# Kernel tuning notes

Hardware: AMD Instinct MI355X
Metric: run time of the kernel (lower is better)

## Reference

```python
import jax, jax.numpy as jnp
import numpy as np

N_EMBD = 2048
N_HEAD = 16
D_HEAD = N_EMBD // N_HEAD  # 128
B, T = 2, 2048
ROPE_BASE = 10000.0


def _rope_cos_sin(T, d, dtype):
    # (T, d) cos/sin tables, rotate-half convention
    inv_freq = 1.0 / (ROPE_BASE ** (jnp.arange(0, d, 2, dtype=jnp.float32) / d))
    ang = jnp.arange(T, dtype=jnp.float32)[:, None] * inv_freq[None, :]  # (T, d/2)
    cos = jnp.concatenate([jnp.cos(ang), jnp.cos(ang)], axis=-1).astype(dtype)
    sin = jnp.concatenate([jnp.sin(ang), jnp.sin(ang)], axis=-1).astype(dtype)
    return cos, sin


def _rotate_half(x):
    d = x.shape[-1] // 2
    return jnp.concatenate([-x[..., d:], x[..., :d]], axis=-1)


def setup_inputs() -> dict:
    key = jax.random.key(0)
    k1, k2, k3 = jax.random.split(key, 3)
    x = jax.random.normal(k1, (B, T, N_EMBD), dtype=jnp.float32)
    w_qkv = jax.random.normal(k2, (3 * N_EMBD, N_EMBD), dtype=jnp.float32) * 0.02
    w_proj = jax.random.normal(k3, (N_EMBD, N_EMBD), dtype=jnp.float32) * 0.02
    return {"x": x, "w_qkv": w_qkv, "w_proj": w_proj}


def reference(x, w_qkv, w_proj):
    Bq, Tq, C = x.shape
    H, D = N_HEAD, D_HEAD
    # fused QKV projection (torch Linear: x @ W.T)
    qkv = jnp.einsum('btc,fc->btf', x, w_qkv).reshape(Bq, Tq, 3, H, D)
    q, k, v = qkv[:, :, 0], qkv[:, :, 1], qkv[:, :, 2]  # (B,T,H,D)
    q = jnp.transpose(q, (0, 2, 1, 3))  # (B,H,T,D)
    k = jnp.transpose(k, (0, 2, 1, 3))
    v = jnp.transpose(v, (0, 2, 1, 3))
    # RoPE (start_pos = 0)
    cos, sin = _rope_cos_sin(Tq, D, x.dtype)  # (T,D)
    q = q * cos[None, None] + _rotate_half(q) * sin[None, None]
    k = k * cos[None, None] + _rotate_half(k) * sin[None, None]
    # causal SDPA
    scale = 1.0 / jnp.sqrt(jnp.asarray(D, x.dtype))
    scores = jnp.einsum('bhqd,bhkd->bhqk', q, k) * scale  # (B,H,T,T)
    causal = jnp.tril(jnp.ones((Tq, Tq), dtype=bool))
    scores = jnp.where(causal[None, None], scores, jnp.asarray(-jnp.inf, x.dtype))
    attn = jax.nn.softmax(scores, axis=-1)
    y = jnp.einsum('bhqk,bhkd->bhqd', attn, v)  # (B,H,T,D)
    y = jnp.transpose(y, (0, 2, 1, 3)).reshape(Bq, Tq, C)
    y = jnp.einsum('btc,fc->btf', y, w_proj)
    return y
```

## Files before the change

### kernel.cpp

```cpp
#include <hip/hip_runtime.h>
#include <hip/hip_bf16.h>
#include <math.h>

typedef __attribute__((ext_vector_type(8))) short short8;
typedef __attribute__((ext_vector_type(4))) short short4_t;
typedef __attribute__((ext_vector_type(4))) float f32x4;

#define Bb 2
#define Tt 2048
#define Hh 16
#define Dd 128
#define Cc 2048
#define Ff 6144

__device__ __forceinline__ size_t packed_idx(int row, int k) {
  return ((((size_t)(row >> 7) * 64 + (k >> 5)) * 8 + ((row >> 4) & 7)) * 512)
         + ((((k >> 3) & 3) * 16 + (row & 15)) * 8) + (k & 7);
}

__device__ __forceinline__ void gload_lds16(const void* g, void* l) {
  __builtin_amdgcn_global_load_lds(
      (const __attribute__((address_space(1))) void*)g,
      (__attribute__((address_space(3))) void*)l, 16, 0, 0);
}

__global__ __launch_bounds__(256) void pack_cast(
    const float* __restrict__ in, __hip_bfloat16* __restrict__ out, int n16)
{
  int t = blockIdx.x * 256 + threadIdx.x;
  if (t >= n16) return;
  int l = t & 63;
  int granule_lin = t >> 6;
  int g = granule_lin & 7;
  int slab = granule_lin >> 3;
  int ks = slab & 63;
  int m_tile = slab >> 6;
  int row = m_tile * 128 + g * 16 + (l & 15);
  int k = ks * 32 + (l >> 4) * 8;
  const float* src = in + (size_t)row * 2048 + k;
  float4 v0 = *(const float4*)src;
  float4 v1 = *(const float4*)(src + 4);
  __hip_bfloat16 tmp[8] = {
      __float2bfloat16(v0.x), __float2bfloat16(v0.y),
      __float2bfloat16(v0.z), __float2bfloat16(v0.w),
      __float2bfloat16(v1.x), __float2bfloat16(v1.y),
      __float2bfloat16(v1.z), __float2bfloat16(v1.w)};
  *(short8*)(out + (size_t)t * 8) = *(const short8*)tmp;
}

__device__ __forceinline__ void store_out(__hip_bfloat16* p, float v) { *p = __float2bfloat16(v); }
__device__ __forceinline__ void store_out(float* p, float v) { *p = v; }

template <typename OutT>
__global__ __launch_bounds__(256) void gemm_pk(
    const __hip_bfloat16* __restrict__ Ap,
    const __hip_bfloat16* __restrict__ Bp,
    OutT* __restrict__ Cm,
    int K, int N)
{
  __shared__ __align__(16) __hip_bfloat16 As[128 * 32];
  __shared__ __align__(16) __hip_bfloat16 Bs[128 * 32];
  const int tid  = threadIdx.x;
  const int wave = tid >> 6;
  const int lane = tid & 63;
  const int quad = lane >> 4;
  const int l16  = lane & 15;
  const int bm = blockIdx.y * 128;
  const int bn = blockIdx.x * 128;
  const int wm4 = (wave >> 1) * 4;
  const int wn4 = (wave & 1) * 4;
  const int KS = K >> 5;

  f32x4 acc[4][4];
#pragma unroll
  for (int i = 0; i < 4; i++)
#pragma unroll
    for (int j = 0; j < 4; j++)
#pragma unroll
      for (int r = 0; r < 4; r++) acc[i][j][r] = 0.f;

  const char* pA[2];
  const char* pB[2];
#pragma unroll
  for (int c = 0; c < 2; c++) {
    int g = wave * 2 + c;
    pA[c] = (const char*)Ap + (size_t)(bm >> 7) * KS * 8192 + g * 1024 + lane * 16;
    pB[c] = (const char*)Bp + (size_t)(bn >> 7) * KS * 8192 + g * 1024 + lane * 16;
  }

  for (int ks = 0; ks < KS; ks++) {
#pragma unroll
    for (int c = 0; c < 2; c++) {
      int g = wave * 2 + c;
      gload_lds16(pA[c], As + g * 512);
      gload_lds16(pB[c], Bs + g * 512);
      pA[c] += 8192;
      pB[c] += 8192;
    }
    __syncthreads();
    short8 af[4], bf[4];
#pragma unroll
    for (int i = 0; i < 4; i++)
      af[i] = *(const short8*)(As + (wm4 + i) * 512 + lane * 8);
#pragma unroll
    for (int j = 0; j < 4; j++)
      bf[j] = *(const short8*)(Bs + (wn4 + j) * 512 + lane * 8);
#pragma unroll
    for (int i = 0; i < 4; i++)
#pragma unroll
      for (int j = 0; j < 4; j++)
        acc[i][j] = __builtin_amdgcn_mfma_f32_16x16x32_bf16(af[i], bf[j], acc[i][j], 0, 0, 0);
    __syncthreads();
  }

#pragma unroll
  for (int i = 0; i < 4; i++)
#pragma unroll
    for (int j = 0; j < 4; j++)
#pragma unroll
      for (int r = 0; r < 4; r++) {
        int gm = bm + (wave >> 1) * 64 + i * 16 + quad * 4 + r;
        int gn = bn + (wave & 1) * 64 + j * 16 + l16;
        store_out(Cm + (size_t)gm * N + gn, acc[i][j][r]);
      }
}

#define GEMM8_PHASE(MB)                                                        \
  {                                                                            \
    short8 af[2][2];                                                           \
    _Pragma("unroll") for (int i = 0; i < 2; i++)                              \
      _Pragma("unroll") for (int k2 = 0; k2 < 2; k2++)                         \
        af[i][k2] = *(const short8*)(Ard + (k2 * 8 + MB + i) * 512 + lane * 8);\
    __builtin_amdgcn_s_barrier();                                              \
    __builtin_amdgcn_s_setprio(1);                                             \
    _Pragma("unroll") for (int i = 0; i < 2; i++)                              \
      _Pragma("unroll") for (int j = 0; j < 4; j++)                            \
        _Pragma("unroll") for (int k2 = 0; k2 < 2; k2++)                       \
          acc[MB + i][j] = __builtin_amdgcn_mfma_f32_16x16x32_bf16(            \
              af[i][k2], bf[j][k2], acc[MB + i][j], 0, 0, 0);                  \
    __builtin_amdgcn_s_setprio(0);                                             \
    __builtin_amdgcn_s_barrier();                                              \
  }

__global__ __launch_bounds__(512, 2) void gemm_pk8(
    const __hip_bfloat16* __restrict__ Ap,
    const __hip_bfloat16* __restrict__ Bp,
    __hip_bfloat16* __restrict__ Cm, int N)
{
  __shared__ __align__(16) __hip_bfloat16 L[65536];
  const int tid  = threadIdx.x;
  const int wave = tid >> 6;
  const int lane = tid & 63;
  const int quad = lane >> 4;
  const int l16  = lane & 15;
  const int wm = wave >> 2;
  const int wn = wave & 3;
  const int bm = blockIdx.y * 256;
  const int bn = blockIdx.x * 256;
  const int NT = 32;
  const int gl = wave * 2;
  const int rb = (wn & 1) * 4;

  const char* pA[2][2];
  const char* pB[2][2];
#pragma unroll
  for (int hh = 0; hh < 2; hh++)
#pragma unroll
    for (int c = 0; c < 2; c++) {
      int g = gl + c;
      pA[hh][c] = (const char*)Ap +
          (size_t)(((bm >> 7) + hh) * 64 + (g >> 3)) * 8192 + (g & 7) * 1024 + lane * 16;
      pB[hh][c] = (const char*)Bp +
          (size_t)(((bn >> 7) + hh) * 64 + (g >> 3)) * 8192 + (g & 7) * 1024 + lane * 16;
    }

#pragma unroll
  for (int hh = 0; hh < 2; hh++) {
#pragma unroll
    for (int c = 0; c < 2; c++)
      gload_lds16(pA[hh][c], &L[hh * 16384 + (gl + c) * 512]);
#pragma unroll
    for (int c = 0; c < 2; c++)
      gload_lds16(pB[hh][c], &L[hh * 16384 + 8192 + (gl + c) * 512]);
  }
#pragma unroll
  for (int hh = 0; hh < 2; hh++)
#pragma unroll
    for (int c = 0; c < 2; c++) { pA[hh][c] += 16384; pB[hh][c] += 16384; }

  f32x4 acc[8][4];
#pragma unroll
  for (int i = 0; i < 8; i++)
#pragma unroll
    for (int j = 0; j < 4; j++)
#pragma unroll
      for (int r = 0; r < 4; r++) acc[i][j][r] = 0.f;

#pragma unroll 1
  for (int t = 0; t < NT; ++t) {
    const int tp = t & 1;
    const __hip_bfloat16* Ard = &L[(wm + 2 * tp) * 16384];
    const __hip_bfloat16* Brd = &L[((wn >> 1) + 2 * tp) * 16384 + 8192];
    __hip_bfloat16* wrA0 = &L[(2 - 2 * tp) * 16384];
    __hip_bfloat16* wrB0 = wrA0 + 8192;
    __hip_bfloat16* wrA1 = wrA0 + 16384;
    __hip_bfloat16* wrB1 = wrA1 + 8192;
    const bool pre = (t + 1 < NT);

    if (pre) {
      gload_lds16(pA[0][0], wrA0 + (gl + 0) * 512);
      gload_lds16(pA[0][1], wrA0 + (gl + 1) * 512);
      __builtin_amdgcn_s_waitcnt(0xF72);
    } else {
      __builtin_amdgcn_s_waitcnt(0xF70);
    }
    __builtin_amdgcn_s_barrier();

    short8 bf[4][2];
#pragma unroll
    for (int j = 0; j < 4; j++)
#pragma unroll
      for (int k2 = 0; k2 < 2; k2++)
        bf[j][k2] = *(const short8*)(Brd + (k2 * 8 + rb + j) * 512 + lane * 8);
    {
      short8 af[2][2];
#pragma unroll
      for (int i = 0; i < 2; i++)
#pragma unroll
        for (int k2 = 0; k2 < 2; k2++)
          af[i][k2] = *(const short8*)(Ard + (k2 * 8 + i) * 512 + lane * 8);
      __builtin_amdgcn_s_setprio(1);
#pragma unroll
      for (int i = 0; i < 2; i++)
#pragma unroll
        for (int j = 0; j < 4; j++)
#pragma unroll
          for (int k2 = 0; k2 < 2; k2++)
            acc[i][j] = __builtin_amdgcn_mfma_f32_16x16x32_bf16(
                af[i][k2], bf[j][k2], acc[i][j], 0, 0, 0);
      __builtin_amdgcn_s_setprio(0);
    }
    __builtin_amdgcn_s_barrier();

    if (pre) {
      gload_lds16(pB[0][0], wrB0 + (gl + 0) * 512);
      gload_lds16(pB[0][1], wrB0 + (gl + 1) * 512);
    }
    GEMM8_PHASE(2);

    if (pre) {
      gload_lds16(pA[1][0], wrA1 + (gl + 0) * 512);
      gload_lds16(pA[1][1], wrA1 + (gl + 1) * 512);
    }
    GEMM8_PHASE(4);

    if (pre) {
      gload_lds16(pB[1][0], wrB1 + (gl + 0) * 512);
      gload_lds16(pB[1][1], wrB1 + (gl + 1) * 512);
    }
    GEMM8_PHASE(6);

    if (pre) {
#pragma unroll
      for (int hh = 0; hh < 2; hh++)
#pragma unroll
        for (int c = 0; c < 2; c++) { pA[hh][c] += 16384; pB[hh][c] += 16384; }
    }
  }

#pragma unroll
  for (int i = 0; i < 8; i++)
#pragma unroll
    for (int j = 0; j < 4; j++)
#pragma unroll
      for (int r = 0; r < 4; r++) {
        int gm = bm + wm * 128 + i * 16 + quad * 4 + r;
        int gn = bn + wn * 64 + j * 16 + l16;
        Cm[(size_t)gm * N + gn] = __float2bfloat16(acc[i][j][r]);
      }
}

__global__ __launch_bounds__(256) void rope_qk(__hip_bfloat16* __restrict__ qkv)
{
  int tid = blockIdx.x * 256 + threadIdx.x;
  int d = tid & 63;
  int h = (tid >> 6) & 15;
  int t = (tid >> 10) & 2047;
  int bw = tid >> 21;
  int b = bw & 1, which = bw >> 1;
  size_t base = (size_t)(b * Tt + t) * Ff + which * 2048 + h * Dd + d;
  float inv = expf(-(float)d * (9.210340371976184f / 64.0f));
  float ang = (float)t * inv;
  float c = cosf(ang), s = sinf(ang);
  float x1 = __bfloat162float(qkv[base]);
  float x2 = __bfloat162float(qkv[base + 64]);
  float o1 = x1 * c - x2 * s;
  float o2 = x2 * c + x1 * s;
  if (which == 0) {
    o1 *= 0.08838834764831845f;
    o2 *= 0.08838834764831845f;
  }
  qkv[base]      = __float2bfloat16(o1);
  qkv[base + 64] = __float2bfloat16(o2);
}

__global__ __launch_bounds__(256) void transpose_v(
    const __hip_bfloat16* __restrict__ qkv, __hip_bfloat16* __restrict__ vt)
{
  __shared__ __hip_bfloat16 tile[64 * 65];
  int bh = blockIdx.y;
  int dt = blockIdx.x >> 5;
  int tt = blockIdx.x & 31;
  int b = bh >> 4, h = bh & 15;
  const __hip_bfloat16* src = qkv + (size_t)(b * Tt + tt * 64) * Ff + 4096 + h * Dd + dt * 64;
#pragma unroll
  for (int i = 0; i < 16; i++) {
    int lin = i * 256 + threadIdx.x;
    int tl = lin >> 6, dc = lin & 63;
    tile[tl * 65 + dc] = src[(size_t)tl * Ff + dc];
  }
  __syncthreads();
  __hip_bfloat16* dst = vt + ((size_t)bh * Dd + dt * 64) * Tt + tt * 64;
#pragma unroll
  for (int i = 0; i < 16; i++) {
    int lin = i * 256 + threadIdx.x;
    int dr = lin >> 6, tc = lin & 63;
    dst[(size_t)dr * Tt + tc] = tile[tc * 65 + dr];
  }
}

__global__ __launch_bounds__(512) void flash_attn3(
    const __hip_bfloat16* __restrict__ qkv,
    const __hip_bfloat16* __restrict__ vt,
    __hip_bfloat16* __restrict__ yat)
{
  __shared__ __align__(16) __hip_bfloat16 KsBuf[2][8192];
  __shared__ __align__(16) __hip_bfloat16 VsBuf[8192];
  __shared__ __align__(16) __hip_bfloat16 PsBuf[8 * 1088];
  const int tid  = threadIdx.x;
  const int wave = tid >> 6;
  const int lane = tid & 63;
  const int quad = lane >> 4;
  const int l16  = lane & 15;
  const int idx  = blockIdx.x;
  const int top  = idx >> 8;
  const int rest = idx & 255;
  const int p    = rest >> 5;
  const int bh   = rest & 31;
  const int qi   = top ? (15 - p) : p;
  const int b = bh >> 4, h = bh & 15;

  const char* kbase = (const char*)(qkv + (size_t)b * Tt * Ff + 2048 + h * Dd);
  const char* vbase = (const char*)(vt + (size_t)bh * Dd * Tt);
  __hip_bfloat16* Pw = PsBuf + wave * 1088;
  const int srow = lane & 15;
  const int scol = lane >> 4;

  const int qm0 = qi * 128;
  const int niter = 2 * qi + 2;

  short8 qf[4];
  {
    const __hip_bfloat16* qrow =
        qkv + (size_t)(b * Tt + qm0 + wave * 16 + l16) * Ff + h * Dd;
#pragma unroll
    for (int kc = 0; kc < 4; kc++)
      qf[kc] = *(const short8*)(qrow + kc * 32 + quad * 8);
  }

#pragma unroll
  for (int c = 0; c < 2; c++) {
    int chunk = wave * 2 + c;
    int j = chunk >> 2, kc = chunk & 3;
    const char* src = kbase + (size_t)(j * 16 + srow) * (Ff * 2) + kc * 64 + scol * 16;
    gload_lds16(src, KsBuf[0] + chunk * 512);
  }

  f32x4 oacc[8];
#pragma unroll
  for (int jd = 0; jd < 8; jd++)
#pragma unroll
    for (int r = 0; r < 4; r++) oacc[jd][r] = 0.f;
  float mrow[4], lrow[4];
#pragma unroll
  for (int r = 0; r < 4; r++) { mrow[r] = -INFINITY; lrow[r] = 0.f; }

#pragma unroll 1
  for (int kt = 0; kt < niter; ++kt) {
    __builtin_amdgcn_s_barrier();
#pragma unroll
    for (int c = 0; c < 2; c++) {
      int chunk = wave * 2 + c;
      int jd = chunk >> 1, k2 = chunk & 1;
      const char* src = vbase + (size_t)(jd * 16 + srow) * (Tt * 2) + kt * 128 + k2 * 64 + scol * 16;
      gload_lds16(src, VsBuf + chunk * 512);
    }
    if (kt + 1 < niter) {
#pragma unroll
      for (int c = 0; c < 2; c++) {
        int chunk = wave * 2 + c;
        int j = chunk >> 2, kc = chunk & 3;
        const char* src = kbase + (size_t)((kt + 1) * 64 + j * 16 + srow) * (Ff * 2) + kc * 64 + scol * 16;
        gload_lds16(src, KsBuf[(kt + 1) & 1] + chunk * 512);
      }
      __builtin_amdgcn_s_waitcnt(0xF74);
    } else {
      __builtin_amdgcn_s_waitcnt(0xF72);
    }
    __builtin_amdgcn_s_barrier();

    const __hip_bfloat16* KsB = KsBuf[kt & 1];
    const bool diag = (kt >= 2 * qi);

    f32x4 sacc[4];
#pragma unroll
    for (int j = 0; j < 4; j++)
#pragma unroll
      for (int r = 0; r < 4; r++) sacc[j][r] = 0.f;
#pragma unroll
    for (int j = 0; j < 4; j++)
#pragma unroll
      for (int kc = 0; kc < 4; kc++) {
        short8 kf = *(const short8*)(KsB + (j * 4 + kc) * 512 + lane * 8);
        sacc[j] = __builtin_amdgcn_mfma_f32_16x16x32_bf16(qf[kc], kf, sacc[j], 0, 0, 0);
      }
    float sv[4][4];
#pragma unroll
    for (int j = 0; j < 4; j++)
#pragma unroll
      for (int r = 0; r < 4; r++) {
        float v = sacc[j][r];
        if (diag) {
          int kg = kt * 64 + j * 16 + l16;
          int qg = qm0 + wave * 16 + quad * 4 + r;
          if (kg > qg) v = -INFINITY;
        }
        sv[j][r] = v;
      }
    float mnew[4];
#pragma unroll
    for (int r = 0; r < 4; r++)
      mnew[r] = fmaxf(fmaxf(sv[0][r], sv[1][r]), fmaxf(sv[2][r], sv[3][r]));
#pragma unroll
    for (int off = 1; off < 16; off <<= 1)
#pragma unroll
      for (int r = 0; r < 4; r++)
        mnew[r] = fmaxf(mnew[r], __shfl_xor(mnew[r], off, 64));
    float alpha[4];
#pragma unroll
    for (int r = 0; r < 4; r++) {
      float mi = fmaxf(mrow[r], mnew[r]);
      alpha[r] = __expf(mrow[r] - mi);
      mrow[r] = mi;
    }
    float rs[4] = {0.f, 0.f, 0.f, 0.f};
#pragma unroll
    for (int j = 0; j < 4; j++)
#pragma unroll
      for (int r = 0; r < 4; r++) {
        float p2 = __expf(sv[j][r] - mrow[r]);
        rs[r] += p2;
        Pw[(j * 2 + (l16 >> 3)) * 136 + (quad * 4 + r) * 8 + (l16 & 7)] = __float2bfloat16(p2);
      }
#pragma unroll
    for (int off = 1; off < 16; off <<= 1)
#pragma unroll
      for (int r = 0; r < 4; r++)
        rs[r] += __shfl_xor(rs[r], off, 64);
#pragma unroll
    for (int r = 0; r < 4; r++) lrow[r] = lrow[r] * alpha[r] + rs[r];
#pragma unroll
    for (int jd = 0; jd < 8; jd++)
#pragma unroll
      for (int r = 0; r < 4; r++) oacc[jd][r] *= alpha[r];

    if (kt + 1 < niter) {
      __builtin_amdgcn_s_waitcnt(0xF72);
    } else {
      __builtin_amdgcn_s_waitcnt(0xF70);
    }
    __builtin_amdgcn_s_barrier();

#pragma unroll
    for (int k2 = 0; k2 < 2; k2++) {
      short8 pf = *(const short8*)(Pw + (k2 * 4 + quad) * 136 + l16 * 8);
#pragma unroll
      for (int jd = 0; jd < 8; jd++) {
        short8 vf = *(const short8*)(VsBuf + (jd * 2 + k2) * 512 + lane * 8);
        oacc[jd] = __builtin_amdgcn_mfma_f32_16x16x32_bf16(pf, vf, oacc[jd], 0, 0, 0);
      }
    }
  }

  float linv[4];
#pragma unroll
  for (int r = 0; r < 4; r++) linv[r] = 1.f / lrow[r];
#pragma unroll
  for (int jd = 0; jd < 8; jd++)
#pragma unroll
    for (int r = 0; r < 4; r++) {
      int row = b * Tt + qm0 + wave * 16 + quad * 4 + r;
      int c = h * Dd + jd * 16 + l16;
      yat[packed_idx(row, c)] = __float2bfloat16(oacc[jd][r] * linv[r]);
    }
}

extern "C" void kernel_launch(void* const* d_in, const int* in_sizes, int n_in,
                              void* d_out, int out_size, void* d_ws, size_t ws_size,
                              hipStream_t stream) {
  (void)in_sizes; (void)n_in; (void)out_size; (void)ws_size;
  const float* x_f      = (const float*)d_in[0];
  const float* w_qkv_f  = (const float*)d_in[1];
  const float* w_proj_f = (const float*)d_in[2];
  float* out = (float*)d_out;

  char* ws = (char*)d_ws;
  __hip_bfloat16* qkv = (__hip_bfloat16*)ws;
  __hip_bfloat16* vt  = (__hip_bfloat16*)(ws + 50331648);
  __hip_bfloat16* yat = (__hip_bfloat16*)(ws + 67108864);
  __hip_bfloat16* xb  = (__hip_bfloat16*)(ws + 83886080);
  __hip_bfloat16* wqb = (__hip_bfloat16*)(ws + 100663296);
  __hip_bfloat16* wpb = (__hip_bfloat16*)(ws + 125829120);

  pack_cast<<<4096, 256, 0, stream>>>(x_f, xb, 1048576);
  pack_cast<<<6144, 256, 0, stream>>>(w_qkv_f, wqb, 1572864);
  pack_cast<<<2048, 256, 0, stream>>>(w_proj_f, wpb, 524288);

  gemm_pk8<<<dim3(24, 16), 512, 0, stream>>>(xb, wqb, qkv, 6144);
  rope_qk<<<32768, 256, 0, stream>>>(qkv);
  transpose_v<<<dim3(64, 32), 256, 0, stream>>>(qkv, vt);
  flash_attn3<<<512, 512, 0, stream>>>(qkv, vt, yat);
  gemm_pk<float><<<dim3(16, 32), 256, 0, stream>>>(yat, wpb, out, 2048, 2048);
}
```

Measured before the change: 437.6 us.

## Rewrite flash attention to load K/V directly into registers with paired query tiles

The attention kernel no longer stages K and V through double-buffered LDS with barriers. Each wave now loads its K and V MFMA fragments straight from global memory into registers, and only the P tile stays in LDS. Blocks shrink to 4 waves over 64-row query tiles, and each block processes a light and a heavy causal tile (p and 31-p) in turn to balance work. This removes LDS traffic and block-wide syncs, but every wave now reads K/V separately, so global/L2 traffic rises and register pressure grows.

```diff
diff --git a/kernel.cpp b/kernel.cpp
--- a/kernel.cpp
+++ b/kernel.cpp
@@ -329,180 +329,151 @@
   }
 }
 
-__global__ __launch_bounds__(512) void flash_attn3(
+__global__ __launch_bounds__(256) void flash_attn4(
     const __hip_bfloat16* __restrict__ qkv,
     const __hip_bfloat16* __restrict__ vt,
     __hip_bfloat16* __restrict__ yat)
 {
-  __shared__ __align__(16) __hip_bfloat16 KsBuf[2][8192];
-  __shared__ __align__(16) __hip_bfloat16 VsBuf[8192];
-  __shared__ __align__(16) __hip_bfloat16 PsBuf[8 * 1088];
+  __shared__ __align__(16) __hip_bfloat16 PsBuf[4 * 1088];
   const int tid  = threadIdx.x;
   const int wave = tid >> 6;
   const int lane = tid & 63;
   const int quad = lane >> 4;
   const int l16  = lane & 15;
-  const int idx  = blockIdx.x;
-  const int top  = idx >> 8;
-  const int rest = idx & 255;
-  const int p    = rest >> 5;
-  const int bh   = rest & 31;
-  const int qi   = top ? (15 - p) : p;
+  const int p  = blockIdx.x >> 5;
+  const int bh = blockIdx.x & 31;
   const int b = bh >> 4, h = bh & 15;
 
-  const char* kbase = (const char*)(qkv + (size_t)b * Tt * Ff + 2048 + h * Dd);
-  const char* vbase = (const char*)(vt + (size_t)bh * Dd * Tt);
+  const char* kb = (const char*)(qkv + (size_t)b * Tt * Ff + 2048 + h * Dd)
+                   + (size_t)l16 * (Ff * 2) + quad * 16;
+  const char* vb = (const char*)(vt + (size_t)bh * Dd * Tt)
+                   + (size_t)l16 * (Tt * 2) + quad * 16;
   __hip_bfloat16* Pw = PsBuf + wave * 1088;
-  const int srow = lane & 15;
-  const int scol = lane >> 4;
-
-  const int qm0 = qi * 128;
-  const int niter = 2 * qi + 2;
-
-  short8 qf[4];
-  {
-    const __hip_bfloat16* qrow =
-        qkv + (size_t)(b * Tt + qm0 + wave * 16 + l16) * Ff + h * Dd;
-#pragma unroll
-    for (int kc = 0; kc < 4; kc++)
-      qf[kc] = *(const short8*)(qrow + kc * 32 + quad * 8);
-  }
-
-#pragma unroll
-  for (int c = 0; c < 2; c++) {
-    int chunk = wave * 2 + c;
-    int j = chunk >> 2, kc = chunk & 3;
-    const char* src = kbase + (size_t)(j * 16 + srow) * (Ff * 2) + kc * 64 + scol * 16;
-    gload_lds16(src, KsBuf[0] + chunk * 512);
-  }
-
-  f32x4 oacc[8];
-#pragma unroll
-  for (int jd = 0; jd < 8; jd++)
-#pragma unroll
-    for (int r = 0; r < 4; r++) oacc[jd][r] = 0.f;
-  float mrow[4], lrow[4];
-#pragma unroll
-  for (int r = 0; r < 4; r++) { mrow[r] = -INFINITY; lrow[r] = 0.f; }
 
 #pragma unroll 1
-  for (int kt = 0; kt < niter; ++kt) {
-    __builtin_amdgcn_s_barrier();
-#pragma unroll
-    for (int c = 0; c < 2; c++) {
-      int chunk = wave * 2 + c;
-      int jd = chunk >> 1, k2 = chunk & 1;
-      const char* src = vbase + (size_t)(jd * 16 + srow) * (Tt * 2) + kt * 128 + k2 * 64 + scol * 16;
-      gload_lds16(src, VsBuf + chunk * 512);
-    }
-    if (kt + 1 < niter) {
-#pragma unroll
-      for (int c = 0; c < 2; c++) {
-        int chunk = wave * 2 + c;
-        int j = chunk >> 2, kc = chunk & 3;
-        const char* src = kbase + (size_t)((kt + 1) * 64 + j * 16 + srow) * (Ff * 2) + kc * 64 + scol * 16;
-        gload_lds16(src, KsBuf[(kt + 1) & 1] + chunk * 512);
+  for (int half = 0; half < 2; ++half) {
+    const int qi = half ? (31 - p) : p;
+    const int qm0 = qi * 64;
+    const int niter = qi + 1;
+
+    short8 qf[4];
+    {
+      const __hip_bfloat16* qrow =
+          qkv + (size_t)(b * Tt + qm0 + wave * 16 + l16) * Ff + h * Dd;
+#pragma unroll
+      for (int kc = 0; kc < 4; kc++)
+        qf[kc] = *(const short8*)(qrow + kc * 32 + quad * 8);
+    }
+
+    f32x4 oacc[8];
+#pragma unroll
+    for (int jd = 0; jd < 8; jd++)
+#pragma unroll
+      for (int r = 0; r < 4; r++) oacc[jd][r] = 0.f;
+    float mrow[4], lrow[4];
+#pragma unroll
+    for (int r = 0; r < 4; r++) { mrow[r] = -INFINITY; lrow[r] = 0.f; }
+
+#pragma unroll 1
+    for (int kt = 0; kt < niter; ++kt) {
+      const char* kbt = kb + (size_t)kt * 64 * (Ff * 2);
+      short8 kf[4][4];
+#pragma unroll
+      for (int j = 0; j < 4; j++)
+#pragma unroll
+        for (int kc = 0; kc < 4; kc++)
+          kf[j][kc] = *(const short8*)(kbt + (size_t)j * (16 * Ff * 2) + kc * 64);
+
+      f32x4 sacc[4];
+#pragma unroll
+      for (int j = 0; j < 4; j++) {
+#pragma unroll
+        for (int r = 0; r < 4; r++) sacc[j][r] = 0.f;
+#pragma unroll
+        for (int kc = 0; kc < 4; kc++)
+          sacc[j] = __builtin_amdgcn_mfma_f32_16x16x32_bf16(qf[kc], kf[j][kc], sacc[j], 0, 0, 0);
       }
-      __builtin_amdgcn_s_waitcnt(0xF74);
-    } else {
-      __builtin_amdgcn_s_waitcnt(0xF72);
-    }
-    __builtin_amdgcn_s_barrier();
-
-    const __hip_bfloat16* KsB = KsBuf[kt & 1];
-    const bool diag = (kt >= 2 * qi);
-
-    f32x4 sacc[4];
-#pragma unroll
-    for (int j = 0; j < 4; j++)
-#pragma unroll
-      for (int r = 0; r < 4; r++) sacc[j][r] = 0.f;
-#pragma unroll
-    for (int j = 0; j < 4; j++)
-#pragma unroll
-      for (int kc = 0; kc < 4; kc++) {
-        short8 kf = *(const short8*)(KsB + (j * 4 + kc) * 512 + lane * 8);
-        sacc[j] = __builtin_amdgcn_mfma_f32_16x16x32_bf16(qf[kc], kf, sacc[j], 0, 0, 0);
+
+      const char* vbt = vb + kt * 128;
+      short8 vf[8][2];
+#pragma unroll
+      for (int jd = 0; jd < 8; jd++)
+#pragma unroll
+        for (int k2 = 0; k2 < 2; k2++)
+          vf[jd][k2] = *(const short8*)(vbt + (size_t)jd * (16 * Tt * 2) + k2 * 64);
+
+      const bool diag = (kt == qi);
+      float sv[4][4];
+#pragma unroll
+      for (int j = 0; j < 4; j++)
+#pragma unroll
+        for (int r = 0; r < 4; r++) {
+          float v = sacc[j][r];
+          if (diag) {
+            int kg = kt * 64 + j * 16 + l16;
+            int qg = qm0 + wave * 16 + quad * 4 + r;
+            if (kg > qg) v = -INFINITY;
+          }
+          sv[j][r] = v;
+        }
+      float mnew[4];
+#pragma unroll
+      for (int r = 0; r < 4; r++)
+        mnew[r] = fmaxf(fmaxf(sv[0][r], sv[1][r]), fmaxf(sv[2][r], sv[3][r]));
+#pragma unroll
+      for (int off = 1; off < 16; off <<= 1)
+#pragma unroll
+        for (int r = 0; r < 4; r++)
+          mnew[r] = fmaxf(mnew[r], __shfl_xor(mnew[r], off, 64));
+      float alpha[4];
+#pragma unroll
+      for (int r = 0; r < 4; r++) {
+        float mi = fmaxf(mrow[r], mnew[r]);
+        alpha[r] = __expf(mrow[r] - mi);
+        mrow[r] = mi;
       }
-    float sv[4][4];
-#pragma unroll
-    for (int j = 0; j < 4; j++)
+      float rs[4] = {0.f, 0.f, 0.f, 0.f};
+#pragma unroll
+      for (int j = 0; j < 4; j++)
+#pragma unroll
+        for (int r = 0; r < 4; r++) {
+          float p2 = __expf(sv[j][r] - mrow[r]);
+          rs[r] += p2;
+          Pw[(j * 2 + (l16 >> 3)) * 136 + (quad * 4 + r) * 8 + (l16 & 7)] = __float2bfloat16(p2);
+        }
+#pragma unroll
+      for (int off = 1; off < 16; off <<= 1)
+#pragma unroll
+        for (int r = 0; r < 4; r++)
+          rs[r] += __shfl_xor(rs[r], off, 64);
+#pragma unroll
+      for (int r = 0; r < 4; r++) lrow[r] = lrow[r] * alpha[r] + rs[r];
+#pragma unroll
+      for (int jd = 0; jd < 8; jd++)
+#pragma unroll
+        for (int r = 0; r < 4; r++) oacc[jd][r] *= alpha[r];
+
+#pragma unroll
+      for (int k2 = 0; k2 < 2; k2++) {
+        short8 pf = *(const short8*)(Pw + (k2 * 4 + quad) * 136 + l16 * 8);
+#pragma unroll
+        for (int jd = 0; jd < 8; jd++)
+          oacc[jd] = __builtin_amdgcn_mfma_f32_16x16x32_bf16(pf, vf[jd][k2], oacc[jd], 0, 0, 0);
+      }
+    }
+
+    float linv[4];
+#pragma unroll
+    for (int r = 0; r < 4; r++) linv[r] = 1.f / lrow[r];
+#pragma unroll
+    for (int jd = 0; jd < 8; jd++)
 #pragma unroll
       for (int r = 0; r < 4; r++) {
-        float v = sacc[j][r];
-        if (diag) {
-          int kg = kt * 64 + j * 16 + l16;
-          int qg = qm0 + wave * 16 + quad * 4 + r;
-          if (kg > qg) v = -INFINITY;
-        }
-        sv[j][r] = v;
+        int row = b * Tt + qm0 + wave * 16 + quad * 4 + r;
+        int c = h * Dd + jd * 16 + l16;
+        yat[packed_idx(row, c)] = __float2bfloat16(oacc[jd][r] * linv[r]);
       }
-    float mnew[4];
-#pragma unroll
-    for (int r = 0; r < 4; r++)
-      mnew[r] = fmaxf(fmaxf(sv[0][r], sv[1][r]), fmaxf(sv[2][r], sv[3][r]));
-#pragma unroll
-    for (int off = 1; off < 16; off <<= 1)
-#pragma unroll
-      for (int r = 0; r < 4; r++)
-        mnew[r] = fmaxf(mnew[r], __shfl_xor(mnew[r], off, 64));
-    float alpha[4];
-#pragma unroll
-    for (int r = 0; r < 4; r++) {
-      float mi = fmaxf(mrow[r], mnew[r]);
-      alpha[r] = __expf(mrow[r] - mi);
-      mrow[r] = mi;
-    }
-    float rs[4] = {0.f, 0.f, 0.f, 0.f};
-#pragma unroll
-    for (int j = 0; j < 4; j++)
-#pragma unroll
-      for (int r = 0; r < 4; r++) {
-        float p2 = __expf(sv[j][r] - mrow[r]);
-        rs[r] += p2;
-        Pw[(j * 2 + (l16 >> 3)) * 136 + (quad * 4 + r) * 8 + (l16 & 7)] = __float2bfloat16(p2);
-      }
-#pragma unroll
-    for (int off = 1; off < 16; off <<= 1)
-#pragma unroll
-      for (int r = 0; r < 4; r++)
-        rs[r] += __shfl_xor(rs[r], off, 64);
-#pragma unroll
-    for (int r = 0; r < 4; r++) lrow[r] = lrow[r] * alpha[r] + rs[r];
-#pragma unroll
-    for (int jd = 0; jd < 8; jd++)
-#pragma unroll
-      for (int r = 0; r < 4; r++) oacc[jd][r] *= alpha[r];
-
-    if (kt + 1 < niter) {
-      __builtin_amdgcn_s_waitcnt(0xF72);
-    } else {
-      __builtin_amdgcn_s_waitcnt(0xF70);
-    }
-    __builtin_amdgcn_s_barrier();
-
-#pragma unroll
-    for (int k2 = 0; k2 < 2; k2++) {
-      short8 pf = *(const short8*)(Pw + (k2 * 4 + quad) * 136 + l16 * 8);
-#pragma unroll
-      for (int jd = 0; jd < 8; jd++) {
-        short8 vf = *(const short8*)(VsBuf + (jd * 2 + k2) * 512 + lane * 8);
-        oacc[jd] = __builtin_amdgcn_mfma_f32_16x16x32_bf16(pf, vf, oacc[jd], 0, 0, 0);
-      }
-    }
-  }
-
-  float linv[4];
-#pragma unroll
-  for (int r = 0; r < 4; r++) linv[r] = 1.f / lrow[r];
-#pragma unroll
-  for (int jd = 0; jd < 8; jd++)
-#pragma unroll
-    for (int r = 0; r < 4; r++) {
-      int row = b * Tt + qm0 + wave * 16 + quad * 4 + r;
-      int c = h * Dd + jd * 16 + l16;
-      yat[packed_idx(row, c)] = __float2bfloat16(oacc[jd][r] * linv[r]);
-    }
+  }
 }
 
 extern "C" void kernel_launch(void* const* d_in, const int* in_sizes, int n_in,
@@ -529,6 +500,6 @@
   gemm_pk8<<<dim3(24, 16), 512, 0, stream>>>(xb, wqb, qkv, 6144);
   rope_qk<<<32768, 256, 0, stream>>>(qkv);
   transpose_v<<<dim3(64, 32), 256, 0, stream>>>(qkv, vt);
-  flash_attn3<<<512, 512, 0, stream>>>(qkv, vt, yat);
+  flash_attn4<<<512, 256, 0, stream>>>(qkv, vt, yat);
   gemm_pk<float><<<dim3(16, 32), 256, 0, stream>>>(yat, wpb, out, 2048, 2048);
 }
```

Result: slower. 561.2 us (+28.2%).
